# Performance work log

Hardware: AMD Instinct MI355X
Metric: run time of the kernel (lower is better)

## Reference

```python
import jax, jax.numpy as jnp
import numpy as np

MARGIN = 1.0

def setup_inputs() -> dict:
    key = jax.random.key(0)
    k1, k2 = jax.random.split(key)
    B, D, NUM_CLASSES = 4096, 512, 64
    inputs = jax.random.normal(k1, (B, D), dtype=jnp.float32)
    labels = jax.random.randint(k2, (B,), 0, NUM_CLASSES, dtype=jnp.int64)
    return {"inputs": inputs, "labels": labels}

def reference(inputs, labels):
    # Full pairwise squared L2 distances via the ||a-b||^2 = ||a||^2 + ||b||^2 - 2 a.b expansion
    sq = jnp.sum(inputs * inputs, axis=1)                      # [B]
    d2 = sq[:, None] + sq[None, :] - 2.0 * (inputs @ inputs.T)  # [B, B]
    d2 = jnp.maximum(d2, 0.0)
    # Safe sqrt: zero (self) distances get exactly 0 without NaN-producing sqrt(0) grads
    nz = d2 > 1e-12
    dist = jnp.where(nz, jnp.sqrt(jnp.where(nz, d2, 1.0)), 0.0)  # [B, B]

    mask = labels[:, None] == labels[None, :]                   # [B, B] same-class mask (includes self)
    mask_f = mask.astype(dist.dtype)

    # Per-anchor: mean distance to positives (self included, contributing 0, as in the torch loop)
    ap_mean = jnp.sum(dist * mask_f, axis=1) / jnp.sum(mask_f, axis=1)  # [B]
    # Per-anchor: min distance to negatives
    an_min = jnp.min(jnp.where(mask, jnp.inf, dist), axis=1)            # [B]

    tmp = ap_mean - an_min + MARGIN                             # [B]
    # `if tmp > 0: loss += tmp` over the batch == sum of relu(tmp)
    return jnp.sum(jnp.maximum(tmp, 0.0))
```

## Files before the change

### kernel.cpp

```cpp
#include <hip/hip_runtime.h>
#include <hip/hip_bf16.h>

typedef unsigned short u16;
typedef unsigned int u32;
typedef __attribute__((ext_vector_type(8))) short short8;
typedef __attribute__((ext_vector_type(8))) u16 ushort8;
typedef __attribute__((ext_vector_type(4))) float f32x4;

#define B_SZ 4096
#define D_SZ 512
#define NCLS 64
#define BK   32
#define NKK  (D_SZ / BK)
#define NT   32
#define NBLK (NT * (NT + 1) / 2)
#define TILE_ELEMS (128 * BK)


__device__ __forceinline__ u16 f2bf(float x) {
    union { float f; u32 u; } a; a.f = x;
    u32 r = a.u + 0x7fffu + ((a.u >> 16) & 1u);
    return (u16)(r >> 16);
}

__device__ __forceinline__ void gload16(const void* g, void* l) {
    __builtin_amdgcn_global_load_lds(
        (const __attribute__((address_space(1))) u32*)g,
        (__attribute__((address_space(3))) u32*)l,
        16, 0, 0);
}

__device__ __forceinline__ void stage_tile32(const u16* __restrict__ gsrc, u16* dst, int t) {
    #pragma unroll
    for (int q = 0; q < 2; ++q) {
        const int s = t + q * 256;
        const int r = s >> 2;
        const int col = ((s & 3) ^ (r & 3)) << 3;
        gload16(gsrc + (size_t)r * D_SZ + col, dst + s * 8);
    }
}


__global__ __launch_bounds__(256) void prep_kernel(
    const float* __restrict__ in, u16* __restrict__ bfout,
    float* __restrict__ sq, float* __restrict__ ap_sum, u32* __restrict__ an_min)
{
    const int wave = threadIdx.x >> 6, l = threadIdx.x & 63;
    const int row = blockIdx.x * 4 + wave;
    const float* p = in + (size_t)row * D_SZ + l * 8;
    float4 v0 = *(const float4*)p;
    float4 v1 = *(const float4*)(p + 4);
    float s = v0.x*v0.x + v0.y*v0.y + v0.z*v0.z + v0.w*v0.w
            + v1.x*v1.x + v1.y*v1.y + v1.z*v1.z + v1.w*v1.w;
    ushort8 o;
    o[0]=f2bf(v0.x); o[1]=f2bf(v0.y); o[2]=f2bf(v0.z); o[3]=f2bf(v0.w);
    o[4]=f2bf(v1.x); o[5]=f2bf(v1.y); o[6]=f2bf(v1.z); o[7]=f2bf(v1.w);
    *(ushort8*)(bfout + (size_t)row * D_SZ + l * 8) = o;
    #pragma unroll
    for (int off = 1; off < 64; off <<= 1) s += __shfl_xor(s, off);
    if (l == 0) {
        sq[row] = s;
        ap_sum[row] = 0.0f;
        an_min[row] = 0x7f800000u;
    }
}


__global__ __launch_bounds__(256) void tile_kernel(
    const u16* __restrict__ bfin, const int* __restrict__ lab,
    const float* __restrict__ sq, float* __restrict__ ap_sum, u32* __restrict__ an_min)
{
    __shared__ u16 As[2][TILE_ELEMS];
    __shared__ u16 Bs[2][TILE_ELEMS];
    __shared__ float sqA[128], sqB[128];
    __shared__ int labA[128], labB[128];

    const int t = threadIdx.x;

    const int bid = blockIdx.x;
    int tm = (int)((__builtin_sqrtf(8.0f * (float)bid + 1.0f) - 1.0f) * 0.5f);
    while ((tm + 1) * (tm + 2) / 2 <= bid) ++tm;
    while (tm * (tm + 1) / 2 > bid) --tm;
    const int tn = bid - tm * (tm + 1) / 2;
    const bool diag = (tm == tn);

    const int rowBase = tm * 128;
    const int colBase = tn * 128;

    if (t < 128) { labA[t] = lab[rowBase + t]; sqA[t] = sq[rowBase + t]; }
    else { int u = t - 128; labB[u] = lab[colBase + u]; sqB[u] = sq[colBase + u]; }

    const int wave = t >> 6, lane = t & 63;
    const int wr = wave >> 1, wc = wave & 1;
    const int g = lane >> 4, c = lane & 15;

    f32x4 acc[4][4];
    #pragma unroll
    for (int i = 0; i < 4; ++i)
        #pragma unroll
        for (int j = 0; j < 4; ++j)
            acc[i][j] = (f32x4){0.f, 0.f, 0.f, 0.f};

    const u16* gA = bfin + (size_t)rowBase * D_SZ;
    const u16* gB = bfin + (size_t)colBase * D_SZ;

    stage_tile32(gA, As[0], t);
    if (!diag) stage_tile32(gB, Bs[0], t);
    __syncthreads();

    const int sw = (g ^ (c & 3)) << 3;

    #pragma unroll 1
    for (int kk = 0; kk < NKK; ++kk) {
        const int cur = kk & 1;
        if (kk + 1 < NKK) {
            stage_tile32(gA + (kk + 1) * BK, As[cur ^ 1], t);
            if (!diag) stage_tile32(gB + (kk + 1) * BK, Bs[cur ^ 1], t);
        }
        const u16* abuf = As[cur];
        const u16* bbuf = diag ? abuf : Bs[cur];

        short8 a[4], b[4];
        #pragma unroll
        for (int mi = 0; mi < 4; ++mi)
            a[mi] = *(const short8*)&abuf[(wr * 64 + mi * 16 + c) * BK + sw];
        #pragma unroll
        for (int ni = 0; ni < 4; ++ni)
            b[ni] = *(const short8*)&bbuf[(wc * 64 + ni * 16 + c) * BK + sw];

        #pragma unroll
        for (int mi = 0; mi < 4; ++mi)
            #pragma unroll
            for (int ni = 0; ni < 4; ++ni)
                acc[mi][ni] = __builtin_amdgcn_mfma_f32_16x16x32_bf16(a[mi], b[ni], acc[mi][ni], 0, 0, 0);

        __syncthreads();
    }

    float sc[4], mc[4];
    #pragma unroll
    for (int ni = 0; ni < 4; ++ni) { sc[ni] = 0.0f; mc[ni] = __builtin_inff(); }

    #pragma unroll
    for (int mi = 0; mi < 4; ++mi) {
        #pragma unroll
        for (int r = 0; r < 4; ++r) {
            const int lrow = wr * 64 + mi * 16 + g * 4 + r;
            const int i = rowBase + lrow;
            const int li = labA[lrow];
            const float sqi = sqA[lrow];
            float s = 0.0f;
            float mn = __builtin_inff();
            #pragma unroll
            for (int ni = 0; ni < 4; ++ni) {
                const int lcol = wc * 64 + ni * 16 + c;
                float d2 = sqi + sqB[lcol] - 2.0f * acc[mi][ni][r];
                d2 = fmaxf(d2, 0.0f);
                float dist = (d2 > 1e-12f) ? __builtin_sqrtf(d2) : 0.0f;
                if (diag && lrow == lcol) dist = 0.0f;
                if (li == labB[lcol]) { s += dist; sc[ni] += dist; }
                else                  { mn = fminf(mn, dist); mc[ni] = fminf(mc[ni], dist); }
            }
            #pragma unroll
            for (int off = 1; off < 16; off <<= 1) {
                s += __shfl_xor(s, off);
                mn = fminf(mn, __shfl_xor(mn, off));
            }
            if (c == 0) {
                atomicAdd(&ap_sum[i], s);
                atomicMin(&an_min[i], __float_as_uint(mn));
            }
        }
    }

    if (!diag) {
        #pragma unroll
        for (int ni = 0; ni < 4; ++ni) {
            float s = sc[ni], mn = mc[ni];
            s += __shfl_xor(s, 16); s += __shfl_xor(s, 32);
            mn = fminf(mn, __shfl_xor(mn, 16)); mn = fminf(mn, __shfl_xor(mn, 32));
            if (lane < 16) {
                const int j = colBase + wc * 64 + ni * 16 + c;
                atomicAdd(&ap_sum[j], s);
                atomicMin(&an_min[j], __float_as_uint(mn));
            }
        }
    }
}


__global__ __launch_bounds__(1024) void final_kernel(
    const float* __restrict__ ap_sum, const u32* __restrict__ an_min,
    const int* __restrict__ lab, float* __restrict__ out)
{
    __shared__ int cnt[NCLS];
    __shared__ float wsum[16];
    const int t = threadIdx.x;
    if (t < NCLS) cnt[t] = 0;
    __syncthreads();
    for (int i = t; i < B_SZ; i += 1024) atomicAdd(&cnt[lab[i]], 1);
    __syncthreads();
    float v = 0.0f;
    for (int i = t; i < B_SZ; i += 1024) {
        float apm = ap_sum[i] / (float)cnt[lab[i]];
        float anm = __uint_as_float(an_min[i]);
        v += fmaxf(apm - anm + 1.0f, 0.0f);
    }
    #pragma unroll
    for (int off = 1; off < 64; off <<= 1) v += __shfl_xor(v, off);
    if ((t & 63) == 0) wsum[t >> 6] = v;
    __syncthreads();
    if (t == 0) {
        float s = 0.0f;
        #pragma unroll
        for (int w = 0; w < 16; ++w) s += wsum[w];
        out[0] = s;
    }
}


extern "C" void kernel_launch(void* const* d_in, const int* in_sizes, int n_in,
                              void* d_out, int out_size, void* d_ws, size_t ws_size,
                              hipStream_t stream) {
    const float* inputs = (const float*)d_in[0];
    const int* labels = (const int*)d_in[1];
    float* out = (float*)d_out;

    char* ws = (char*)d_ws;
    float* ap_sum = (float*)ws;
    u32* an_min = (u32*)(ws + 16384);
    float* sq = (float*)(ws + 32768);
    u16* bfin = (u16*)(ws + 65536);

    prep_kernel<<<dim3(B_SZ / 4), dim3(256), 0, stream>>>(inputs, bfin, sq, ap_sum, an_min);
    tile_kernel<<<dim3(NBLK), dim3(256), 0, stream>>>(bfin, labels, sq, ap_sum, an_min);
    final_kernel<<<dim3(1), dim3(1024), 0, stream>>>(ap_sum, an_min, labels, out);
}
```

Measured before the change: 41.00 us.

## Triple-buffer GEMM loads, swizzle block order, parallelize final reduction

The tile kernel moves from double to triple buffering. It uses explicit vmcnt waits and raw barriers, so two k-slices are in flight and one barrier per iteration goes away; the loop is also fully unrolled. Diagonal blocks now load the B tile redundantly. Block ids are permuted across 8 groups to change the scheduling order. Class counts move into prep_kernel via atomics, and the single-block final kernel becomes 16 blocks that reduce with an atomicAdd into the output, at the cost of an extra memset launch.

```diff
diff --git a/kernel.cpp b/kernel.cpp
--- a/kernel.cpp
+++ b/kernel.cpp
@@ -16,6 +16,10 @@
 #define NBLK (NT * (NT + 1) / 2)
 #define TILE_ELEMS (128 * BK)
 
+#define WAITV4()  asm volatile("s_waitcnt vmcnt(4)" ::: "memory")
+#define WAITV0()  asm volatile("s_waitcnt vmcnt(0)" ::: "memory")
+#define BARRIER() asm volatile("s_barrier" ::: "memory")
+
 
 __device__ __forceinline__ u16 f2bf(float x) {
     union { float f; u32 u; } a; a.f = x;
@@ -42,9 +46,11 @@
 
 
 __global__ __launch_bounds__(256) void prep_kernel(
-    const float* __restrict__ in, u16* __restrict__ bfout,
-    float* __restrict__ sq, float* __restrict__ ap_sum, u32* __restrict__ an_min)
+    const float* __restrict__ in, const int* __restrict__ lab, u16* __restrict__ bfout,
+    float* __restrict__ sq, float* __restrict__ ap_sum, u32* __restrict__ an_min,
+    int* __restrict__ counts, float* __restrict__ out)
 {
+    if (blockIdx.x == 0 && threadIdx.x == 0) out[0] = 0.0f;
     const int wave = threadIdx.x >> 6, l = threadIdx.x & 63;
     const int row = blockIdx.x * 4 + wave;
     const float* p = in + (size_t)row * D_SZ + l * 8;
@@ -62,6 +68,7 @@
         sq[row] = s;
         ap_sum[row] = 0.0f;
         an_min[row] = 0x7f800000u;
+        atomicAdd(&counts[lab[row]], 1);
     }
 }
 
@@ -70,14 +77,16 @@
     const u16* __restrict__ bfin, const int* __restrict__ lab,
     const float* __restrict__ sq, float* __restrict__ ap_sum, u32* __restrict__ an_min)
 {
-    __shared__ u16 As[2][TILE_ELEMS];
-    __shared__ u16 Bs[2][TILE_ELEMS];
+    __shared__ u16 As[3][TILE_ELEMS];
+    __shared__ u16 Bs[3][TILE_ELEMS];
     __shared__ float sqA[128], sqB[128];
     __shared__ int labA[128], labB[128];
 
     const int t = threadIdx.x;
 
-    const int bid = blockIdx.x;
+    int bid = blockIdx.x;
+    bid = (bid & 7) * (NBLK / 8) + (bid >> 3);
+
     int tm = (int)((__builtin_sqrtf(8.0f * (float)bid + 1.0f) - 1.0f) * 0.5f);
     while ((tm + 1) * (tm + 2) / 2 <= bid) ++tm;
     while (tm * (tm + 1) / 2 > bid) --tm;
@@ -104,21 +113,28 @@
     const u16* gA = bfin + (size_t)rowBase * D_SZ;
     const u16* gB = bfin + (size_t)colBase * D_SZ;
 
-    stage_tile32(gA, As[0], t);
-    if (!diag) stage_tile32(gB, Bs[0], t);
     __syncthreads();
 
+    stage_tile32(gA,      As[0], t);
+    stage_tile32(gB,      Bs[0], t);
+    stage_tile32(gA + BK, As[1], t);
+    stage_tile32(gB + BK, Bs[1], t);
+
     const int sw = (g ^ (c & 3)) << 3;
 
-    #pragma unroll 1
+    #pragma unroll
     for (int kk = 0; kk < NKK; ++kk) {
-        const int cur = kk & 1;
-        if (kk + 1 < NKK) {
-            stage_tile32(gA + (kk + 1) * BK, As[cur ^ 1], t);
-            if (!diag) stage_tile32(gB + (kk + 1) * BK, Bs[cur ^ 1], t);
+        if (kk < NKK - 1) { WAITV4(); }
+        else              { WAITV0(); }
+        BARRIER();
+
+        if (kk + 2 < NKK) {
+            stage_tile32(gA + (kk + 2) * BK, As[(kk + 2) % 3], t);
+            stage_tile32(gB + (kk + 2) * BK, Bs[(kk + 2) % 3], t);
         }
-        const u16* abuf = As[cur];
-        const u16* bbuf = diag ? abuf : Bs[cur];
+
+        const u16* abuf = As[kk % 3];
+        const u16* bbuf = Bs[kk % 3];
 
         short8 a[4], b[4];
         #pragma unroll
@@ -133,8 +149,6 @@
             #pragma unroll
             for (int ni = 0; ni < 4; ++ni)
                 acc[mi][ni] = __builtin_amdgcn_mfma_f32_16x16x32_bf16(a[mi], b[ni], acc[mi][ni], 0, 0, 0);
-
-        __syncthreads();
     }
 
     float sc[4], mc[4];
@@ -189,33 +203,21 @@
 }
 
 
-__global__ __launch_bounds__(1024) void final_kernel(
+__global__ __launch_bounds__(256) void final_kernel(
     const float* __restrict__ ap_sum, const u32* __restrict__ an_min,
-    const int* __restrict__ lab, float* __restrict__ out)
+    const int* __restrict__ lab, const int* __restrict__ counts, float* __restrict__ out)
 {
-    __shared__ int cnt[NCLS];
-    __shared__ float wsum[16];
+    __shared__ float wsum[4];
     const int t = threadIdx.x;
-    if (t < NCLS) cnt[t] = 0;
-    __syncthreads();
-    for (int i = t; i < B_SZ; i += 1024) atomicAdd(&cnt[lab[i]], 1);
-    __syncthreads();
-    float v = 0.0f;
-    for (int i = t; i < B_SZ; i += 1024) {
-        float apm = ap_sum[i] / (float)cnt[lab[i]];
-        float anm = __uint_as_float(an_min[i]);
-        v += fmaxf(apm - anm + 1.0f, 0.0f);
-    }
+    const int i = blockIdx.x * 256 + t;
+    float apm = ap_sum[i] / (float)counts[lab[i]];
+    float anm = __uint_as_float(an_min[i]);
+    float v = fmaxf(apm - anm + 1.0f, 0.0f);
     #pragma unroll
     for (int off = 1; off < 64; off <<= 1) v += __shfl_xor(v, off);
     if ((t & 63) == 0) wsum[t >> 6] = v;
     __syncthreads();
-    if (t == 0) {
-        float s = 0.0f;
-        #pragma unroll
-        for (int w = 0; w < 16; ++w) s += wsum[w];
-        out[0] = s;
-    }
+    if (t == 0) atomicAdd(out, wsum[0] + wsum[1] + wsum[2] + wsum[3]);
 }
 
 
@@ -230,9 +232,11 @@
     float* ap_sum = (float*)ws;
     u32* an_min = (u32*)(ws + 16384);
     float* sq = (float*)(ws + 32768);
+    int* counts = (int*)(ws + 49152);
     u16* bfin = (u16*)(ws + 65536);
 
-    prep_kernel<<<dim3(B_SZ / 4), dim3(256), 0, stream>>>(inputs, bfin, sq, ap_sum, an_min);
+    hipMemsetAsync(counts, 0, NCLS * sizeof(int), stream);
+    prep_kernel<<<dim3(B_SZ / 4), dim3(256), 0, stream>>>(inputs, labels, bfin, sq, ap_sum, an_min, counts, out);
     tile_kernel<<<dim3(NBLK), dim3(256), 0, stream>>>(bfin, labels, sq, ap_sum, an_min);
-    final_kernel<<<dim3(1), dim3(1024), 0, stream>>>(ap_sum, an_min, labels, out);
-}
+    final_kernel<<<dim3(B_SZ / 256), dim3(256), 0, stream>>>(ap_sum, an_min, labels, counts, out);
+}
```

New measurement: 60.24 us. 46.9% more time.
